# Kernel optimization log

Hardware: AMD Instinct MI355X
Metric: run time of the kernel (lower is better)

## Reference

```python
import jax, jax.numpy as jnp
import numpy as np

B, S, E, C, H = 64, 2048, 512, 512, 256


def setup_inputs() -> dict:
    key = jax.random.key(0)
    ks = jax.random.split(key, 8)
    encoder_word_embeds = jax.random.normal(ks[0], (B, S, E), dtype=jnp.float32)
    encoder_lengths = jax.random.randint(ks[1], (B,), 1, S + 1)  # lengths in [1, S]
    context_state = jax.random.normal(ks[2], (B, C), dtype=jnp.float32)
    # Learned parameters (nn.Linear style: y = x @ W.T + b)
    sw = 1.0 / np.sqrt(E)
    sc = 1.0 / np.sqrt(C)
    sh = 1.0 / np.sqrt(H)
    W_word = jax.random.uniform(ks[3], (H, E), minval=-sw, maxval=sw, dtype=jnp.float32)
    b_word = jax.random.uniform(ks[4], (H,), minval=-sw, maxval=sw, dtype=jnp.float32)
    W_ctx = jax.random.uniform(ks[5], (H, C), minval=-sc, maxval=sc, dtype=jnp.float32)
    b_ctx = jax.random.uniform(ks[6], (H,), minval=-sc, maxval=sc, dtype=jnp.float32)
    w_hidden = jax.random.uniform(ks[7], (H,), minval=-sh, maxval=sh, dtype=jnp.float32)  # hidden_layer has no bias
    return {
        "encoder_word_embeds": encoder_word_embeds,
        "encoder_lengths": encoder_lengths,
        "context_state": context_state,
        "W_word": W_word,
        "b_word": b_word,
        "W_ctx": W_ctx,
        "b_ctx": b_ctx,
        "w_hidden": w_hidden,
    }


def reference(encoder_word_embeds, encoder_lengths, context_state, W_word, b_word, W_ctx, b_ctx, w_hidden):
    seq_len = encoder_word_embeds.shape[1]
    # word mask [B, S]: positions < length
    positions = jnp.arange(seq_len)  # [S]
    mask = (positions[None, :] < encoder_lengths[:, None]).astype(jnp.float32)  # [B, S]
    # additive attention MLP
    word_feat = jnp.einsum("bse,he->bsh", encoder_word_embeds, W_word) + b_word  # [B,S,H]
    ctx_feat = context_state @ W_ctx.T + b_ctx  # [B,H]
    scores = jnp.einsum("bsh,h->bs", jnp.tanh(word_feat + ctx_feat[:, None, :]), w_hidden)  # [B,S]
    # softmax over seq, then mask and renormalize (matches original order)
    attn = jax.nn.softmax(scores, axis=1) * mask
    attn = attn / (1e-10 + attn.sum(axis=1, keepdims=True))  # [B,S]
    attention_features = jnp.einsum("bs,bse->be", attn, encoder_word_embeds)  # [B,E]
    return attention_features, attn
```

## Files before the change

### kernel.cpp

```cpp
#include <hip/hip_runtime.h>
#include <hip/hip_bf16.h>
#include <cstdint>
#include <cstddef>

#define B_  64
#define S_  2048
#define E_  512
#define C_  512
#define H_  256

using f32x4 = __attribute__((ext_vector_type(4))) float;
using s16x8 = __attribute__((ext_vector_type(8))) short;

__device__ __forceinline__ unsigned short f2bf(float f) {
    union { float f; unsigned u; } v; v.f = f;
    unsigned u = v.u;
    return (unsigned short)((u + 0x7FFFu + ((u >> 16) & 1u)) >> 16);
}

__global__ void prep_w(const float* __restrict__ W, unsigned short* __restrict__ Wb) {
    int i = (blockIdx.x * 256 + threadIdx.x) * 4;
    float4 v = *(const float4*)(W + i);
    ushort4 o; o.x = f2bf(v.x); o.y = f2bf(v.y); o.z = f2bf(v.z); o.w = f2bf(v.w);
    *(ushort4*)(Wb + i) = o;
}

__global__ void prep_ctx(const float* __restrict__ ctx, const float* __restrict__ Wc,
                         const float* __restrict__ bc, const float* __restrict__ bw,
                         float* __restrict__ cb) {
    __shared__ float row[C_];
    int b = blockIdx.x, t = threadIdx.x;
    row[t] = ctx[b * C_ + t];
    row[t + 256] = ctx[b * C_ + t + 256];
    __syncthreads();
    const float4* w4 = (const float4*)(Wc + (size_t)t * C_);
    const float4* x4 = (const float4*)row;
    float acc = 0.f;
    #pragma unroll 4
    for (int c = 0; c < C_ / 4; ++c) {
        float4 w = w4[c], x = x4[c];
        acc += w.x * x.x + w.y * x.y + w.z * x.z + w.w * x.w;
    }
    cb[b * H_ + t] = acc + bc[t] + bw[t];
}

#define BM 128
#define BN 256
#define BK 64
#define LDT 72

__global__ __launch_bounds__(512) void scores_kernel(
    const float* __restrict__ A,
    const unsigned short* __restrict__ Wb,
    const float* __restrict__ cb,
    const float* __restrict__ wh,
    float* __restrict__ scores)
{
    __shared__ __align__(16) unsigned short At[BM * LDT];
    __shared__ __align__(16) unsigned short Bt[BN * LDT];
    __shared__ float sblk[BM];
    int t = threadIdx.x;
    int m0 = blockIdx.x * BM;
    int b  = m0 >> 11;

    int w = t >> 6, lane = t & 63, quad = lane >> 4, lm = lane & 15;
    int wm = (w & 1) * 64, wn = (w >> 1) * 64;

    if (t < BM) sblk[t] = 0.f;

    f32x4 acc[4][4] = {};

    int arow = t >> 4, acol = (t & 15) * 4;
    int brow = t >> 3, bcol = (t & 7) * 8;

    for (int k0 = 0; k0 < E_; k0 += BK) {
        #pragma unroll
        for (int i = 0; i < 4; ++i) {
            int r = arow + i * 32;
            float4 v = *(const float4*)(A + (size_t)(m0 + r) * E_ + k0 + acol);
            ushort4 o; o.x = f2bf(v.x); o.y = f2bf(v.y); o.z = f2bf(v.z); o.w = f2bf(v.w);
            *(ushort4*)(At + r * LDT + acol) = o;
        }
        #pragma unroll
        for (int i = 0; i < 4; ++i) {
            int r = brow + i * 64;
            uint4 v = *(const uint4*)(Wb + (size_t)r * E_ + k0 + bcol);
            *(uint4*)(Bt + r * LDT + bcol) = v;
        }
        __syncthreads();
        #pragma unroll
        for (int ks = 0; ks < 2; ++ks) {
            s16x8 af[4], bfr[4];
            #pragma unroll
            for (int i = 0; i < 4; ++i)
                af[i] = *(const s16x8*)(At + (wm + i * 16 + lm) * LDT + ks * 32 + quad * 8);
            #pragma unroll
            for (int i = 0; i < 4; ++i)
                bfr[i] = *(const s16x8*)(Bt + (wn + i * 16 + lm) * LDT + ks * 32 + quad * 8);
            #pragma unroll
            for (int mi = 0; mi < 4; ++mi)
                #pragma unroll
                for (int ni = 0; ni < 4; ++ni)
                    acc[mi][ni] = __builtin_amdgcn_mfma_f32_16x16x32_bf16(
                        af[mi], bfr[ni], acc[mi][ni], 0, 0, 0);
        }
        __syncthreads();
    }

    float wv[4], cbv[4];
    #pragma unroll
    for (int ni = 0; ni < 4; ++ni) {
        int n = wn + ni * 16 + lm;
        wv[ni]  = wh[n];
        cbv[ni] = cb[b * H_ + n];
    }
    #pragma unroll
    for (int mi = 0; mi < 4; ++mi) {
        #pragma unroll
        for (int r = 0; r < 4; ++r) {
            float p = 0.f;
            #pragma unroll
            for (int ni = 0; ni < 4; ++ni) {
                float x = acc[mi][ni][r] + cbv[ni];
                x = fminf(fmaxf(x, -15.f), 15.f);
                float e = __expf(2.f * x);
                float th = 1.f - 2.f * __builtin_amdgcn_rcpf(e + 1.f);
                p += wv[ni] * th;
            }
            #pragma unroll
            for (int off = 8; off >= 1; off >>= 1)
                p += __shfl_xor(p, off);
            if (lm == 0)
                atomicAdd(&sblk[wm + mi * 16 + quad * 4 + r], p);
        }
    }
    __syncthreads();
    if (t < BM) scores[m0 + t] = sblk[t];
}

__global__ void softmax_kernel(const int* __restrict__ lens, float* __restrict__ attn) {
    __shared__ float redm[4], redz[4], redt[4];
    int b = blockIdx.x, t = threadIdx.x;
    int len = lens[b];
    float* sc = attn + (size_t)b * S_;
    float v[8];
    #pragma unroll
    for (int i = 0; i < 8; ++i) v[i] = sc[t + i * 256];
    float m = -1e30f;
    #pragma unroll
    for (int i = 0; i < 8; ++i) m = fmaxf(m, v[i]);
    #pragma unroll
    for (int off = 32; off >= 1; off >>= 1) m = fmaxf(m, __shfl_xor(m, off));
    if ((t & 63) == 0) redm[t >> 6] = m;
    __syncthreads();
    m = fmaxf(fmaxf(redm[0], redm[1]), fmaxf(redm[2], redm[3]));
    float e[8]; float z = 0.f, tm = 0.f;
    #pragma unroll
    for (int i = 0; i < 8; ++i) {
        e[i] = __expf(v[i] - m);
        z += e[i];
        if (t + i * 256 < len) tm += e[i];
    }
    #pragma unroll
    for (int off = 32; off >= 1; off >>= 1) { z += __shfl_xor(z, off); tm += __shfl_xor(tm, off); }
    if ((t & 63) == 0) { redz[t >> 6] = z; redt[t >> 6] = tm; }
    __syncthreads();
    z  = redz[0] + redz[1] + redz[2] + redz[3];
    tm = redt[0] + redt[1] + redt[2] + redt[3];
    float invZ  = 1.f / z;
    float denom = 1e-10f + tm * invZ;
    float sfac  = invZ / denom;
    #pragma unroll
    for (int i = 0; i < 8; ++i) {
        int s = t + i * 256;
        sc[s] = (s < len) ? e[i] * sfac : 0.f;
    }
}

__global__ void wsum_kernel(const float* __restrict__ A, const float* __restrict__ attn,
                            const int* __restrict__ lens, float* __restrict__ out) {
    int b = blockIdx.y;
    int len = lens[b];
    int s0 = blockIdx.x * 128;
    if (s0 >= len) return;
    int send = s0 + 128; if (send > len) send = len;
    int t = threadIdx.x;
    const float* ap = attn + (size_t)b * S_;
    const float* Ab = A + ((size_t)b * S_ + s0) * E_ + t;
    float acc = 0.f;
    for (int s = s0; s < send; ++s, Ab += E_)
        acc += ap[s] * (*Ab);
    atomicAdd(&out[b * E_ + t], acc);
}

extern "C" void kernel_launch(void* const* d_in, const int* in_sizes, int n_in,
                              void* d_out, int out_size, void* d_ws, size_t ws_size,
                              hipStream_t stream) {
    const float* embeds = (const float*)d_in[0];
    const int*   lens   = (const int*)d_in[1];
    const float* ctx    = (const float*)d_in[2];
    const float* Ww     = (const float*)d_in[3];
    const float* bw     = (const float*)d_in[4];
    const float* Wc     = (const float*)d_in[5];
    const float* bc     = (const float*)d_in[6];
    const float* wh     = (const float*)d_in[7];
    float* out  = (float*)d_out;
    float* feat = out;
    float* attn = out + B_ * E_;

    unsigned short* Wb = (unsigned short*)d_ws;
    float* cb = (float*)((char*)d_ws + (size_t)H_ * E_ * sizeof(unsigned short));

    hipMemsetAsync(feat, 0, (size_t)B_ * E_ * sizeof(float), stream);
    prep_w<<<(H_ * E_) / 1024, 256, 0, stream>>>(Ww, Wb);
    prep_ctx<<<B_, 256, 0, stream>>>(ctx, Wc, bc, bw, cb);
    scores_kernel<<<dim3(B_ * S_ / BM), 512, 0, stream>>>(embeds, Wb, cb, wh, attn);
    softmax_kernel<<<B_, 256, 0, stream>>>(lens, attn);
    wsum_kernel<<<dim3(S_ / 128, B_), 512, 0, stream>>>(embeds, attn, lens, feat);
}
```

Measured before the change: 475.7 us.

## Skip score GEMM tiles beyond sequence length and simplify masked softmax

Score-GEMM blocks whose starting position is at or past the batch row's length now exit early, since masked positions receive zero attention after renormalisation. The softmax is restricted to valid positions, which folds the two normalisations into one and drops a reduction and barrier. The bf16 conversion uses packed intrinsics, and the weighted-sum loop uses four accumulators for more memory-level parallelism. The epsilon in the renormalisation is dropped, which changes results slightly only in degenerate cases.

Result: faster. 429.0 us (-9.8%).

```diff
diff --git a/kernel.cpp b/kernel.cpp
--- a/kernel.cpp
+++ b/kernel.cpp
@@ -18,11 +18,19 @@
     return (unsigned short)((u + 0x7FFFu + ((u >> 16) & 1u)) >> 16);
 }
 
+__device__ __forceinline__ uint2 f4_to_bf4(float4 v) {
+    __hip_bfloat162 lo = __float22bfloat162_rn(make_float2(v.x, v.y));
+    __hip_bfloat162 hi = __float22bfloat162_rn(make_float2(v.z, v.w));
+    union { __hip_bfloat162 b; unsigned u; } a, c;
+    a.b = lo; c.b = hi;
+    return make_uint2(a.u, c.u);
+}
+
 __global__ void prep_w(const float* __restrict__ W, unsigned short* __restrict__ Wb) {
     int i = (blockIdx.x * 256 + threadIdx.x) * 4;
     float4 v = *(const float4*)(W + i);
-    ushort4 o; o.x = f2bf(v.x); o.y = f2bf(v.y); o.z = f2bf(v.z); o.w = f2bf(v.w);
-    *(ushort4*)(Wb + i) = o;
+    uint2 o = f4_to_bf4(v);
+    *(uint2*)(Wb + i) = o;
 }
 
 __global__ void prep_ctx(const float* __restrict__ ctx, const float* __restrict__ Wc,
@@ -54,6 +62,7 @@
     const unsigned short* __restrict__ Wb,
     const float* __restrict__ cb,
     const float* __restrict__ wh,
+    const int*   __restrict__ lens,
     float* __restrict__ scores)
 {
     __shared__ __align__(16) unsigned short At[BM * LDT];
@@ -62,6 +71,8 @@
     int t = threadIdx.x;
     int m0 = blockIdx.x * BM;
     int b  = m0 >> 11;
+    int ms = m0 & (S_ - 1);
+    if (ms >= lens[b]) return;
 
     int w = t >> 6, lane = t & 63, quad = lane >> 4, lm = lane & 15;
     int wm = (w & 1) * 64, wn = (w >> 1) * 64;
@@ -78,8 +89,7 @@
         for (int i = 0; i < 4; ++i) {
             int r = arow + i * 32;
             float4 v = *(const float4*)(A + (size_t)(m0 + r) * E_ + k0 + acol);
-            ushort4 o; o.x = f2bf(v.x); o.y = f2bf(v.y); o.z = f2bf(v.z); o.w = f2bf(v.w);
-            *(ushort4*)(At + r * LDT + acol) = o;
+            *(uint2*)(At + r * LDT + acol) = f4_to_bf4(v);
         }
         #pragma unroll
         for (int i = 0; i < 4; ++i) {
@@ -139,13 +149,16 @@
 }
 
 __global__ void softmax_kernel(const int* __restrict__ lens, float* __restrict__ attn) {
-    __shared__ float redm[4], redz[4], redt[4];
+    __shared__ float redm[4], redt[4];
     int b = blockIdx.x, t = threadIdx.x;
     int len = lens[b];
     float* sc = attn + (size_t)b * S_;
     float v[8];
     #pragma unroll
-    for (int i = 0; i < 8; ++i) v[i] = sc[t + i * 256];
+    for (int i = 0; i < 8; ++i) {
+        int s = t + i * 256;
+        v[i] = (s < len) ? sc[s] : -1e30f;
+    }
     float m = -1e30f;
     #pragma unroll
     for (int i = 0; i < 8; ++i) m = fmaxf(m, v[i]);
@@ -154,26 +167,23 @@
     if ((t & 63) == 0) redm[t >> 6] = m;
     __syncthreads();
     m = fmaxf(fmaxf(redm[0], redm[1]), fmaxf(redm[2], redm[3]));
-    float e[8]; float z = 0.f, tm = 0.f;
-    #pragma unroll
-    for (int i = 0; i < 8; ++i) {
-        e[i] = __expf(v[i] - m);
-        z += e[i];
-        if (t + i * 256 < len) tm += e[i];
-    }
-    #pragma unroll
-    for (int off = 32; off >= 1; off >>= 1) { z += __shfl_xor(z, off); tm += __shfl_xor(tm, off); }
-    if ((t & 63) == 0) { redz[t >> 6] = z; redt[t >> 6] = tm; }
-    __syncthreads();
-    z  = redz[0] + redz[1] + redz[2] + redz[3];
-    tm = redt[0] + redt[1] + redt[2] + redt[3];
-    float invZ  = 1.f / z;
-    float denom = 1e-10f + tm * invZ;
-    float sfac  = invZ / denom;
+    float e[8]; float tm = 0.f;
     #pragma unroll
     for (int i = 0; i < 8; ++i) {
         int s = t + i * 256;
-        sc[s] = (s < len) ? e[i] * sfac : 0.f;
+        e[i] = (s < len) ? __expf(v[i] - m) : 0.f;
+        tm += e[i];
+    }
+    #pragma unroll
+    for (int off = 32; off >= 1; off >>= 1) tm += __shfl_xor(tm, off);
+    if ((t & 63) == 0) redt[t >> 6] = tm;
+    __syncthreads();
+    tm = redt[0] + redt[1] + redt[2] + redt[3];
+    float sfac = 1.f / tm;
+    #pragma unroll
+    for (int i = 0; i < 8; ++i) {
+        int s = t + i * 256;
+        sc[s] = e[i] * sfac;
     }
 }
 
@@ -187,10 +197,16 @@
     int t = threadIdx.x;
     const float* ap = attn + (size_t)b * S_;
     const float* Ab = A + ((size_t)b * S_ + s0) * E_ + t;
-    float acc = 0.f;
-    for (int s = s0; s < send; ++s, Ab += E_)
-        acc += ap[s] * (*Ab);
-    atomicAdd(&out[b * E_ + t], acc);
+    float a0 = 0.f, a1 = 0.f, a2 = 0.f, a3 = 0.f;
+    int s = s0;
+    for (; s + 3 < send; s += 4, Ab += 4 * E_) {
+        a0 += ap[s + 0] * Ab[0 * E_];
+        a1 += ap[s + 1] * Ab[1 * E_];
+        a2 += ap[s + 2] * Ab[2 * E_];
+        a3 += ap[s + 3] * Ab[3 * E_];
+    }
+    for (; s < send; ++s, Ab += E_) a0 += ap[s] * (*Ab);
+    atomicAdd(&out[b * E_ + t], (a0 + a1) + (a2 + a3));
 }
 
 extern "C" void kernel_launch(void* const* d_in, const int* in_sizes, int n_in,
@@ -214,7 +230,7 @@
     hipMemsetAsync(feat, 0, (size_t)B_ * E_ * sizeof(float), stream);
     prep_w<<<(H_ * E_) / 1024, 256, 0, stream>>>(Ww, Wb);
     prep_ctx<<<B_, 256, 0, stream>>>(ctx, Wc, bc, bw, cb);
-    scores_kernel<<<dim3(B_ * S_ / BM), 512, 0, stream>>>(embeds, Wb, cb, wh, attn);
+    scores_kernel<<<dim3(B_ * S_ / BM), 512, 0, stream>>>(embeds, Wb, cb, wh, lens, attn);
     softmax_kernel<<<B_, 256, 0, stream>>>(lens, attn);
     wsum_kernel<<<dim3(S_ / 128, B_), 512, 0, stream>>>(embeds, attn, lens, feat);
 }
```
